# Kernel tuning notes

Measured on AMD Instinct MI355X. Metric: run time of the kernel, lower is better.

The kernel has to match this reference:

```python
import jax, jax.numpy as jnp
import numpy as np

SIZE = 4096
NB = 16            # nr_blocks_per_row
NDROP = 8          # nr_blocks_to_drop_per_row
BATCH = 8192
BLOCK = SIZE // NB # 256


def _block_mask():
    # latin_square(n): S[i,j] = ((i+j) mod n) + 1, values 1..n, each once per row/col
    i = np.arange(NB)
    S = ((i[:, None] + i[None, :]) % NB) + 1
    m = S > NDROP  # keep NB-NDROP blocks per row
    mask = np.repeat(np.repeat(m, BLOCK, axis=0), BLOCK, axis=1)
    return jnp.asarray(mask)  # [SIZE, SIZE] bool


def setup_inputs() -> dict:
    key = jax.random.key(0)
    kx, kw, kb = jax.random.split(key, 3)
    x = jax.random.normal(kx, (BATCH, SIZE), dtype=jnp.float32)
    # kaiming_normal_ default: fan_in mode, relu gain -> std = sqrt(2/fan_in)
    weight = jax.random.normal(kw, (SIZE, SIZE), dtype=jnp.float32) * jnp.sqrt(2.0 / SIZE)
    # uniform(-1,1) scaled by sqrt(1/size)
    bias = jax.random.uniform(kb, (SIZE,), minval=-1.0, maxval=1.0, dtype=jnp.float32) * jnp.sqrt(1.0 / SIZE)
    mask = _block_mask()
    return {"x": x, "weight": weight, "bias": bias, "mask": mask}


def reference(x, weight, bias, mask):
    # x @ (mask * weight).T + bias
    w = jnp.where(mask, weight, jnp.zeros((), dtype=weight.dtype))
    return x @ w.T + bias
```

## Files before the change

kernel.cpp:

```cpp
#include <hip/hip_runtime.h>
#include <hip/hip_bf16.h>
#include <stdint.h>


typedef __bf16 bf16x8 __attribute__((ext_vector_type(8)));
typedef float  f32x4  __attribute__((ext_vector_type(4)));

#define AS1 __attribute__((address_space(1)))
#define AS3 __attribute__((address_space(3)))

__device__ __forceinline__ void async_cp16(const void* g, void* l) {
  __builtin_amdgcn_global_load_lds((const AS1 void*)g, (AS3 void*)l, 16, 0, 0);
}

__device__ __forceinline__ uint32_t pack_bf16(float a, float b) {
  uint32_t ua = __float_as_uint(a);
  ua += 0x7fffu + ((ua >> 16) & 1u);
  uint32_t ub = __float_as_uint(b);
  ub += 0x7fffu + ((ub >> 16) & 1u);
  return (ua >> 16) | (ub & 0xffff0000u);
}

__global__ __launch_bounds__(256) void cvt_x(const float* __restrict__ x,
                                             uint2* __restrict__ xb) {
  const int t = threadIdx.x;
  const int b = blockIdx.x;
  const float4* p = (const float4*)(x + (size_t)b * 4096);
  uint2* o = xb + (size_t)b * 1024;
  float4 a0 = p[t];
  float4 a1 = p[t + 256];
  float4 a2 = p[t + 512];
  float4 a3 = p[t + 768];
  o[t]       = make_uint2(pack_bf16(a0.x, a0.y), pack_bf16(a0.z, a0.w));
  o[t + 256] = make_uint2(pack_bf16(a1.x, a1.y), pack_bf16(a1.z, a1.w));
  o[t + 512] = make_uint2(pack_bf16(a2.x, a2.y), pack_bf16(a2.z, a2.w));
  o[t + 768] = make_uint2(pack_bf16(a3.x, a3.y), pack_bf16(a3.z, a3.w));
}

__global__ __launch_bounds__(256) void cvt_w(const float* __restrict__ w,
                                             uint2* __restrict__ wb) {
  const int t = threadIdx.x;
  const int n = blockIdx.x;
  const int kstart = ((8 - (n >> 8)) & 15) << 8;
  const float* src = w + (size_t)n * 4096;
  uint2* dst = wb + (size_t)n * 512;
  float4 a0 = *(const float4*)(src + ((kstart + 4 * t) & 4095));
  float4 a1 = *(const float4*)(src + ((kstart + 1024 + 4 * t) & 4095));
  dst[t]       = make_uint2(pack_bf16(a0.x, a0.y), pack_bf16(a0.z, a0.w));
  dst[t + 256] = make_uint2(pack_bf16(a1.x, a1.y), pack_bf16(a1.z, a1.w));
}

__global__ __launch_bounds__(512, 2) void gemm_bs8(
    const uint16_t* __restrict__ X,
    const uint16_t* __restrict__ W,
    const float* __restrict__ bias,
    float* __restrict__ out) {
  __shared__ char L[131072];

  const int tid = threadIdx.x;
  const int lin = blockIdx.x;
  const int xcd = lin & 7;
  const int idx = lin >> 3;
  const int bm = idx >> 1;
  const int bn = (xcd << 1) + (idx & 1);
  const int m0 = bm << 8;
  const int n0 = bn << 8;
  const int kstart = ((8 - bn) & 15) << 8;

  const int chswz = (((tid & 7) ^ ((tid >> 4) & 7)) << 3);
  const uint16_t* Xb = X + (size_t)(m0 + (tid >> 3)) * 4096 + chswz;
  const uint16_t* Wb = W + (size_t)(n0 + ((tid >> 8) << 6) + ((tid >> 3) & 31)) * 2048 + chswz;
  char* dA = L + tid * 16;
  char* dB = L + 32768 + tid * 16;

  auto stageA = [&](int buf, int q, int s) {
    const size_t gk = (size_t)((kstart + (s << 6)) & 4095);
    const uint16_t* s0 = Xb + (size_t)(q << 6) * 4096 + gk;
    char* d = dA + (buf << 16) + (q << 13);
    async_cp16(s0, d);
    async_cp16(s0 + (size_t)128 * 4096, d + 16384);
  };
  auto stageB = [&](int buf, int b, int s) {
    const uint16_t* s0 = Wb + (size_t)(b << 5) * 2048 + (s << 6);
    char* d = dB + (buf << 16) + (b << 14);
    async_cp16(s0, d);
    async_cp16(s0 + (size_t)128 * 2048, d + 8192);
  };

  const int lane = tid & 63;
  const int wv = tid >> 6;
  const int wmh = wv >> 2;
  const int wnq = wv & 3;
  const int fr = lane & 15;
  const int g = lane >> 4;
  const int fsw = (fr >> 1) & 7;
  const int sl0 = ((g ^ fsw) << 4);
  const int sl1 = (((g + 4) ^ fsw) << 4);
  const int aoff = wmh * 16384 + fr * 128;
  const int boff = 32768 + wnq * 4096 + fr * 128;

  f32x4 acc[8][4];
#pragma unroll
  for (int i = 0; i < 8; ++i)
#pragma unroll
    for (int j = 0; j < 4; ++j)
      acc[i][j] = (f32x4){0.f, 0.f, 0.f, 0.f};

#define VMW(N) asm volatile("s_waitcnt vmcnt(" #N ")" ::: "memory")

#define PHASE(BUF, QM, QN, WAITSTMT, STAGE)                                   \
  {                                                                           \
    const int ab = ((BUF) << 16) + aoff + (QM) * 8192;                        \
    const int bb = ((BUF) << 16) + boff + (QN) * 16384;                       \
    bf16x8 av[4][2], bv[2][2];                                                \
    _Pragma("unroll")                                                         \
    for (int i = 0; i < 4; ++i) {                                             \
      av[i][0] = *(const bf16x8*)(L + ab + i * 2048 + sl0);                   \
      av[i][1] = *(const bf16x8*)(L + ab + i * 2048 + sl1);                   \
    }                                                                         \
    _Pragma("unroll")                                                         \
    for (int j = 0; j < 2; ++j) {                                             \
      bv[j][0] = *(const bf16x8*)(L + bb + j * 2048 + sl0);                   \
      bv[j][1] = *(const bf16x8*)(L + bb + j * 2048 + sl1);                   \
    }                                                                         \
    STAGE;                                                                    \
    __builtin_amdgcn_s_barrier();                                             \
    asm volatile("s_waitcnt lgkmcnt(0)" ::: "memory");                        \
    __builtin_amdgcn_sched_barrier(0);                                        \
    __builtin_amdgcn_s_setprio(1);                                            \
    _Pragma("unroll")                                                         \
    for (int i = 0; i < 4; ++i)                                               \
      _Pragma("unroll")                                                       \
      for (int j = 0; j < 2; ++j) {                                           \
        acc[(QM) * 4 + i][(QN) * 2 + j] =                                     \
            __builtin_amdgcn_mfma_f32_16x16x32_bf16(                          \
                av[i][0], bv[j][0], acc[(QM) * 4 + i][(QN) * 2 + j], 0, 0, 0);\
        acc[(QM) * 4 + i][(QN) * 2 + j] =                                     \
            __builtin_amdgcn_mfma_f32_16x16x32_bf16(                          \
                av[i][1], bv[j][1], acc[(QM) * 4 + i][(QN) * 2 + j], 0, 0, 0);\
      }                                                                       \
    __builtin_amdgcn_s_setprio(0);                                            \
    WAITSTMT;                                                                 \
    __builtin_amdgcn_s_barrier();                                             \
  }

  stageA(0, 0, 0);
  stageB(0, 0, 0);
  stageB(0, 1, 0);
  stageA(0, 1, 0);
  asm volatile("s_waitcnt vmcnt(0)" ::: "memory");
  __builtin_amdgcn_s_barrier();

  for (int t = 0; t < 31; ++t) {
    const int buf = t & 1;
    const int nb = buf ^ 1;
    const int s1 = t + 1;
    PHASE(buf, 0, 0, VMW(4), stageA(nb, 0, s1));
    PHASE(buf, 0, 1, VMW(4), stageB(nb, 0, s1));
    PHASE(buf, 1, 0, (void)0, stageB(nb, 1, s1));
    PHASE(buf, 1, 1, VMW(4), stageA(nb, 1, s1));
  }
  PHASE(1, 0, 0, VMW(2), (void)0);
  PHASE(1, 0, 1, VMW(0), (void)0);
  PHASE(1, 1, 0, (void)0, (void)0);
  PHASE(1, 1, 1, (void)0, (void)0);
#undef PHASE
#undef VMW

  const int rq = g << 2;
#pragma unroll
  for (int j = 0; j < 4; ++j) {
    const int c = n0 + wnq * 64 + ((j >> 1) << 5) + ((j & 1) << 4) + fr;
    const float bz = bias[c];
#pragma unroll
    for (int i = 0; i < 8; ++i) {
      const int r0 = m0 + wmh * 128 + ((i >> 2) << 6) + ((i & 3) << 4) + rq;
#pragma unroll
      for (int r = 0; r < 4; ++r)
        out[(size_t)(r0 + r) * 4096 + c] = acc[i][j][r] + bz;
    }
  }
}

extern "C" void kernel_launch(void* const* d_in, const int* in_sizes, int n_in,
                              void* d_out, int out_size, void* d_ws, size_t ws_size,
                              hipStream_t stream) {
  const float* x = (const float*)d_in[0];
  const float* w = (const float*)d_in[1];
  const float* bias = (const float*)d_in[2];
  float* out = (float*)d_out;

  uint16_t* xb = (uint16_t*)d_ws;
  uint16_t* wb = xb + (size_t)8192 * 4096;

  hipLaunchKernelGGL(cvt_x, dim3(8192), dim3(256), 0, stream, x, (uint2*)xb);
  hipLaunchKernelGGL(cvt_w, dim3(4096), dim3(256), 0, stream, w, (uint2*)wb);

  hipLaunchKernelGGL(gemm_bs8, dim3(512), dim3(512), 0, stream,
                     xb, wb, bias, out);
}
```

Before: 430.1 us.

## Switch GEMM to 32x32x16 MFMA tiles with two-phase pipeline per k-step

Replaces the 16x16x32 bf16 MFMA micro-tiles with 32x32x16 MFMA, changing the LDS fragment layout, the swizzle, and the accumulator shape. Each k-step now runs two phases instead of four. A fragments are loaded once and reused across both N halves, and each phase stages a full A or B tile. This is meant to cut LDS reads and barriers per MFMA and to use the larger MFMA shape's better operand reuse. In exchange, register pressure rises from holding av[4][4], and the epilogue store pattern changes.

```diff
diff --git a/kernel.cpp b/kernel.cpp
--- a/kernel.cpp
+++ b/kernel.cpp
@@ -4,7 +4,7 @@
 
 
 typedef __bf16 bf16x8 __attribute__((ext_vector_type(8)));
-typedef float  f32x4  __attribute__((ext_vector_type(4)));
+typedef float  f32x16 __attribute__((ext_vector_type(16)));
 
 #define AS1 __attribute__((address_space(1)))
 #define AS3 __attribute__((address_space(3)))
@@ -67,117 +67,112 @@
   const int n0 = bn << 8;
   const int kstart = ((8 - bn) & 15) << 8;
 
-  const int chswz = (((tid & 7) ^ ((tid >> 4) & 7)) << 3);
-  const uint16_t* Xb = X + (size_t)(m0 + (tid >> 3)) * 4096 + chswz;
-  const uint16_t* Wb = W + (size_t)(n0 + ((tid >> 8) << 6) + ((tid >> 3) & 31)) * 2048 + chswz;
+  const int trow = tid >> 3;
+  const int chswz = (((tid & 7) ^ (trow & 7)) << 3);
+  const uint16_t* Xa = X + (size_t)(m0 + trow) * 4096 + chswz;
+  const uint16_t* Wa = W + (size_t)(n0 + trow) * 2048 + chswz;
   char* dA = L + tid * 16;
   char* dB = L + 32768 + tid * 16;
 
-  auto stageA = [&](int buf, int q, int s) {
-    const size_t gk = (size_t)((kstart + (s << 6)) & 4095);
-    const uint16_t* s0 = Xb + (size_t)(q << 6) * 4096 + gk;
-    char* d = dA + (buf << 16) + (q << 13);
-    async_cp16(s0, d);
-    async_cp16(s0 + (size_t)128 * 4096, d + 16384);
+  auto stageA = [&](int buf, int s) {
+    const int kb = (kstart + (s << 6)) & 4095;
+    const uint16_t* p = Xa + kb;
+    char* d = dA + (buf << 16);
+#pragma unroll
+    for (int c = 0; c < 4; ++c)
+      async_cp16(p + (size_t)(c << 6) * 4096, d + (c << 13));
   };
-  auto stageB = [&](int buf, int b, int s) {
-    const uint16_t* s0 = Wb + (size_t)(b << 5) * 2048 + (s << 6);
-    char* d = dB + (buf << 16) + (b << 14);
-    async_cp16(s0, d);
-    async_cp16(s0 + (size_t)128 * 2048, d + 8192);
+  auto stageB = [&](int buf, int s) {
+    const uint16_t* p = Wa + (s << 6);
+    char* d = dB + (buf << 16);
+#pragma unroll
+    for (int c = 0; c < 4; ++c)
+      async_cp16(p + (size_t)(c << 6) * 2048, d + (c << 13));
   };
 
   const int lane = tid & 63;
   const int wv = tid >> 6;
   const int wmh = wv >> 2;
   const int wnq = wv & 3;
-  const int fr = lane & 15;
-  const int g = lane >> 4;
-  const int fsw = (fr >> 1) & 7;
-  const int sl0 = ((g ^ fsw) << 4);
-  const int sl1 = (((g + 4) ^ fsw) << 4);
-  const int aoff = wmh * 16384 + fr * 128;
-  const int boff = 32768 + wnq * 4096 + fr * 128;
+  const int cl = lane & 31;
+  const int g01 = lane >> 5;
+  const int lx7 = lane & 7;
+  int sl[4];
+#pragma unroll
+  for (int s = 0; s < 4; ++s) sl[s] = (((2 * s + g01) ^ lx7) << 4);
+  const int aoff = (wmh * 128 + cl) * 128;
+  const int boff = 32768 + (wnq * 64 + cl) * 128;
 
-  f32x4 acc[8][4];
+  f32x16 acc[4][2];
 #pragma unroll
-  for (int i = 0; i < 8; ++i)
+  for (int i = 0; i < 4; ++i)
 #pragma unroll
-    for (int j = 0; j < 4; ++j)
-      acc[i][j] = (f32x4){0.f, 0.f, 0.f, 0.f};
+    for (int j = 0; j < 2; ++j)
+#pragma unroll
+      for (int e = 0; e < 16; ++e) acc[i][j][e] = 0.f;
+
+  bf16x8 av[4][4];
+  bf16x8 bv[4];
 
 #define VMW(N) asm volatile("s_waitcnt vmcnt(" #N ")" ::: "memory")
 
-#define PHASE(BUF, QM, QN, WAITSTMT, STAGE)                                   \
+#define PHASE(BUFB, QN, DOA, WAITSTMT, STAGE)                                 \
   {                                                                           \
-    const int ab = ((BUF) << 16) + aoff + (QM) * 8192;                        \
-    const int bb = ((BUF) << 16) + boff + (QN) * 16384;                       \
-    bf16x8 av[4][2], bv[2][2];                                                \
-    _Pragma("unroll")                                                         \
-    for (int i = 0; i < 4; ++i) {                                             \
-      av[i][0] = *(const bf16x8*)(L + ab + i * 2048 + sl0);                   \
-      av[i][1] = *(const bf16x8*)(L + ab + i * 2048 + sl1);                   \
+    if (DOA) {                                                                \
+      _Pragma("unroll")                                                       \
+      for (int i = 0; i < 4; ++i)                                             \
+        _Pragma("unroll")                                                     \
+        for (int s = 0; s < 4; ++s)                                           \
+          av[i][s] = *(const bf16x8*)(L + (BUFB) + aoff + i * 4096 + sl[s]);  \
     }                                                                         \
     _Pragma("unroll")                                                         \
-    for (int j = 0; j < 2; ++j) {                                             \
-      bv[j][0] = *(const bf16x8*)(L + bb + j * 2048 + sl0);                   \
-      bv[j][1] = *(const bf16x8*)(L + bb + j * 2048 + sl1);                   \
-    }                                                                         \
+    for (int s = 0; s < 4; ++s)                                               \
+      bv[s] = *(const bf16x8*)(L + (BUFB) + boff + (QN) * 4096 + sl[s]);      \
     STAGE;                                                                    \
     __builtin_amdgcn_s_barrier();                                             \
     asm volatile("s_waitcnt lgkmcnt(0)" ::: "memory");                        \
     __builtin_amdgcn_sched_barrier(0);                                        \
     __builtin_amdgcn_s_setprio(1);                                            \
     _Pragma("unroll")                                                         \
-    for (int i = 0; i < 4; ++i)                                               \
+    for (int s = 0; s < 4; ++s)                                               \
       _Pragma("unroll")                                                       \
-      for (int j = 0; j < 2; ++j) {                                           \
-        acc[(QM) * 4 + i][(QN) * 2 + j] =                                     \
-            __builtin_amdgcn_mfma_f32_16x16x32_bf16(                          \
-                av[i][0], bv[j][0], acc[(QM) * 4 + i][(QN) * 2 + j], 0, 0, 0);\
-        acc[(QM) * 4 + i][(QN) * 2 + j] =                                     \
-            __builtin_amdgcn_mfma_f32_16x16x32_bf16(                          \
-                av[i][1], bv[j][1], acc[(QM) * 4 + i][(QN) * 2 + j], 0, 0, 0);\
-      }                                                                       \
+      for (int i = 0; i < 4; ++i)                                             \
+        acc[i][QN] = __builtin_amdgcn_mfma_f32_32x32x16_bf16(                 \
+            av[i][s], bv[s], acc[i][QN], 0, 0, 0);                            \
     __builtin_amdgcn_s_setprio(0);                                            \
     WAITSTMT;                                                                 \
     __builtin_amdgcn_s_barrier();                                             \
   }
 
-  stageA(0, 0, 0);
-  stageB(0, 0, 0);
-  stageB(0, 1, 0);
-  stageA(0, 1, 0);
+  stageA(0, 0);
+  stageB(0, 0);
   asm volatile("s_waitcnt vmcnt(0)" ::: "memory");
   __builtin_amdgcn_s_barrier();
 
   for (int t = 0; t < 31; ++t) {
-    const int buf = t & 1;
-    const int nb = buf ^ 1;
-    const int s1 = t + 1;
-    PHASE(buf, 0, 0, VMW(4), stageA(nb, 0, s1));
-    PHASE(buf, 0, 1, VMW(4), stageB(nb, 0, s1));
-    PHASE(buf, 1, 0, (void)0, stageB(nb, 1, s1));
-    PHASE(buf, 1, 1, VMW(4), stageA(nb, 1, s1));
+    const int bufb = (t & 1) << 16;
+    const int nb = (t & 1) ^ 1;
+    PHASE(bufb, 0, 1, VMW(4), stageA(nb, t + 1));
+    PHASE(bufb, 1, 0, VMW(2), stageB(nb, t + 1));
   }
-  PHASE(1, 0, 0, VMW(2), (void)0);
-  PHASE(1, 0, 1, VMW(0), (void)0);
-  PHASE(1, 1, 0, (void)0, (void)0);
-  PHASE(1, 1, 1, (void)0, (void)0);
+  PHASE((1 << 16), 0, 1, VMW(0), (void)0);
+  PHASE((1 << 16), 1, 0, (void)0, (void)0);
 #undef PHASE
 #undef VMW
 
-  const int rq = g << 2;
+  const int r4 = g01 << 2;
 #pragma unroll
-  for (int j = 0; j < 4; ++j) {
-    const int c = n0 + wnq * 64 + ((j >> 1) << 5) + ((j & 1) << 4) + fr;
+  for (int j = 0; j < 2; ++j) {
+    const int c = n0 + wnq * 64 + (j << 5) + cl;
     const float bz = bias[c];
 #pragma unroll
-    for (int i = 0; i < 8; ++i) {
-      const int r0 = m0 + wmh * 128 + ((i >> 2) << 6) + ((i & 3) << 4) + rq;
+    for (int i = 0; i < 4; ++i) {
+      const int rb = m0 + wmh * 128 + (i << 5) + r4;
 #pragma unroll
-      for (int r = 0; r < 4; ++r)
-        out[(size_t)(r0 + r) * 4096 + c] = acc[i][j][r] + bz;
+      for (int reg = 0; reg < 16; ++reg) {
+        const int r = rb + (reg & 3) + ((reg >> 2) << 3);
+        out[(size_t)r * 4096 + c] = acc[i][j][reg] + bz;
+      }
     }
   }
 }
```

Measured after the change: 440.7 us. +2.5%, slower.
